# Optimization experiments

Hardware: AMD Instinct MI355X
Metric: run time of the kernel (lower is better)

## Reference

```python
import jax, jax.numpy as jnp
import numpy as np

N_NODES = 50000
N_EDGES = 800000
D_IN = 128
D_OUT = 128


def setup_inputs() -> dict:
    key = jax.random.key(0)
    k1, k2, k3, k4, k5, k6 = jax.random.split(key, 6)
    feat = jax.random.normal(k1, (N_NODES, D_IN), dtype=jnp.float32)
    src = jax.random.randint(k2, (N_EDGES,), 0, N_NODES, dtype=jnp.int64)
    dst = jax.random.randint(k3, (N_EDGES,), 0, N_NODES, dtype=jnp.int64)
    edge_weight = jax.random.uniform(k4, (N_EDGES,), dtype=jnp.float32)
    W_neigh = jax.random.normal(k5, (D_OUT, D_IN), dtype=jnp.float32) * (1.0 / np.sqrt(D_IN))
    W_self = jax.random.normal(k6, (D_OUT, D_IN), dtype=jnp.float32) * (1.0 / np.sqrt(D_IN))
    b_self = jnp.zeros((D_OUT,), dtype=jnp.float32)
    return {"feat": feat, "src": src, "dst": dst, "edge_weight": edge_weight,
            "W_neigh": W_neigh, "W_self": W_self, "b_self": b_self}


def reference(feat, src, dst, edge_weight, W_neigh, W_self, b_self):
    n_nodes = feat.shape[0]
    # fc_neigh on source features: [N, D_out]
    h = feat @ W_neigh.T
    # per-edge weighted messages: m_e = h[src_e] * w_e  -> [E, D_out]
    msg = h[src] * edge_weight[:, None]
    # mean aggregation over incoming edges (0 for isolated dst nodes, as DGL)
    neigh_sum = jax.ops.segment_sum(msg, dst, num_segments=n_nodes)
    deg = jax.ops.segment_sum(jnp.ones_like(edge_weight), dst, num_segments=n_nodes)
    neigh = neigh_sum / jnp.maximum(deg, 1.0)[:, None]
    # fc_self residual path + neighborhood term
    out = feat @ W_self.T + b_self + neigh
    return out
```

## Files before the change

### kernel.cpp

```cpp
#include <hip/hip_runtime.h>

#define CAP 32
#define OVFCAP 65536
#define BSTRIDE 5120
#define BINCHUNK 4096

typedef __attribute__((ext_vector_type(8))) short bf16x8;
typedef __attribute__((ext_vector_type(4))) float f32x4;

__device__ __forceinline__ unsigned f2bf(float x) {
  unsigned u = __float_as_uint(x);
  return (u + 0x7fffu + ((u >> 16) & 1u)) >> 16;
}

__device__ __forceinline__ bf16x8 u4_to_bf(uint4 v) {
  union { uint4 u; bf16x8 b; } cv;
  cv.u = v;
  return cv.b;
}

__global__ __launch_bounds__(512) void zero_kernel(int* __restrict__ p) {
  if (threadIdx.x < 257) p[threadIdx.x] = 0;
}

__global__ __launch_bounds__(256) void prep_kernel(
    const int* __restrict__ src, const int* __restrict__ dst,
    const float* __restrict__ ew, int* __restrict__ gbin,
    uint2* __restrict__ binbuf, int* __restrict__ ovfcnt,
    uint2* __restrict__ ovf, int E,
    const float* __restrict__ feat, unsigned* __restrict__ fb,
    unsigned* __restrict__ fbq, int total4,
    const float* __restrict__ Ws, const float* __restrict__ Wn,
    unsigned* __restrict__ wsb, unsigned* __restrict__ wnb,
    int nchunk) {
  __shared__ int lcnt[256];
  __shared__ int lbase[256];
  const int b = blockIdx.x;
  const int tid = threadIdx.x;
  if (b < nchunk) {
    lcnt[tid] = 0;
    __syncthreads();
    const int e0 = b * BINCHUNK;
    const int e1 = min(E, e0 + BINCHUNK);
    int dreg[BINCHUNK / 256];
#pragma unroll
    for (int i = 0; i < BINCHUNK / 256; ++i) {
      const int e = e0 + i * 256 + tid;
      dreg[i] = (e < e1) ? dst[e] : -1;
      if (dreg[i] >= 0) atomicAdd(&lcnt[dreg[i] >> 8], 1);
    }
    __syncthreads();
    lbase[tid] = lcnt[tid] ? atomicAdd(&gbin[tid], lcnt[tid]) : 0;
    lcnt[tid] = 0;
    __syncthreads();
#pragma unroll
    for (int i = 0; i < BINCHUNK / 256; ++i) {
      const int e = e0 + i * 256 + tid;
      if (e < e1) {
        const int d = dreg[i];
        const int bn = d >> 8;
        const int r = atomicAdd(&lcnt[bn], 1);
        const int pos = lbase[bn] + r;
        const uint2 rec = make_uint2(((unsigned)d << 16) | (unsigned)src[e],
                                     __float_as_uint(ew[e]));
        if (pos < BSTRIDE) {
          binbuf[(size_t)bn * BSTRIDE + pos] = rec;
        } else {
          int p = atomicAdd(ovfcnt, 1);
          if (p < OVFCAP) ovf[p] = rec;
        }
      }
    }
  } else if (b < nchunk + 1024) {
    const int bid = b - nchunk;
    for (int i = bid * 256 + tid; i < total4; i += 1024 * 256) {
      float4 v = ((const float4*)feat)[i];
      fb[2 * i] = f2bf(v.x) | (f2bf(v.y) << 16);
      fb[2 * i + 1] = f2bf(v.z) | (f2bf(v.w) << 16);
      unsigned q = 0;
      q = __builtin_amdgcn_cvt_pk_fp8_f32(v.x, v.y, q, false);
      q = __builtin_amdgcn_cvt_pk_fp8_f32(v.z, v.w, q, true);
      fbq[i] = q;
    }
  } else {
    const int i = (b - nchunk - 1024) * 256 + tid;
    if (i < 8192) {
      float2 a = ((const float2*)Ws)[i];
      wsb[i] = f2bf(a.x) | (f2bf(a.y) << 16);
      float2 v = ((const float2*)Wn)[i];
      wnb[i] = f2bf(v.x) | (f2bf(v.y) << 16);
    }
  }
}

__global__ __launch_bounds__(256) void bucket_kernel(
    const int* __restrict__ gbin, const uint2* __restrict__ binbuf,
    int* __restrict__ cnt, unsigned* __restrict__ colw,
    int* __restrict__ ovfcnt, uint2* __restrict__ ovf, int n) {
  __shared__ uint4 lbucket4[256 * CAP / 4];
  __shared__ int lcnt[256];
  unsigned* lbucket = (unsigned*)lbucket4;
  const int b = blockIdx.x;
  const int tid = threadIdx.x;
  lcnt[tid] = 0;
  __syncthreads();
  const int lo = b << 8;
  const int m = min(gbin[b], BSTRIDE);
  const uint2* bb = binbuf + (size_t)b * BSTRIDE;
  for (int i = tid; i < m; i += 256) {
    const uint2 rec = bb[i];
    const int dl = (int)(rec.x >> 16) & 255;
    const int r = atomicAdd(&lcnt[dl], 1);
    if (r < CAP) {
      const float w = __uint_as_float(rec.y);
      const unsigned q = (unsigned)(w * 65535.0f + 0.5f);
      lbucket[dl * CAP + r] = ((rec.x & 0xffffu) << 16) | q;
    } else {
      int p = atomicAdd(ovfcnt, 1);
      if (p < OVFCAP) ovf[p] = rec;
    }
  }
  __syncthreads();
  const int nn = min(256, n - lo);
  if (tid < nn) cnt[lo + tid] = lcnt[tid];
  const int tot4 = (nn * CAP) >> 2;
  uint4* d4 = (uint4*)(colw + (size_t)lo * CAP);
  for (int i = tid; i < tot4; i += 256) d4[i] = lbucket4[i];
}

__global__ __launch_bounds__(256) void gather_kernel(
    const unsigned* __restrict__ fbq, const int* __restrict__ cnt,
    const unsigned* __restrict__ colw, const int* __restrict__ ovfcnt,
    const uint2* __restrict__ ovf, unsigned* __restrict__ aggu, int n) {
  const int wid = (blockIdx.x * 256 + threadIdx.x) >> 6;
  const int lane = threadIdx.x & 63;
  if (wid >= n) return;
  const int g = lane >> 5;
  const int sl = lane & 31;
  const int dg = cnt[wid];
  const int m = min(dg, CAP);
  const unsigned pv = (lane < m) ? colw[(size_t)wid * CAP + lane] : 0u;
  float a0 = 0.f, a1 = 0.f, a2 = 0.f, a3 = 0.f;
  const float qs = 1.0f / 65535.0f;
  int t = 0;
  for (; t + 16 <= m; t += 16) {
    unsigned p[8], u[8];
#pragma unroll
    for (int i = 0; i < 8; ++i) p[i] = __shfl(pv, t + 2 * i + g);
#pragma unroll
    for (int i = 0; i < 8; ++i) u[i] = fbq[(size_t)(p[i] >> 16) * 32 + sl];
#pragma unroll
    for (int i = 0; i < 8; ++i) {
      const float w = (float)(p[i] & 0xffffu) * qs;
      a0 += __builtin_amdgcn_cvt_f32_fp8(u[i], 0) * w;
      a1 += __builtin_amdgcn_cvt_f32_fp8(u[i], 1) * w;
      a2 += __builtin_amdgcn_cvt_f32_fp8(u[i], 2) * w;
      a3 += __builtin_amdgcn_cvt_f32_fp8(u[i], 3) * w;
    }
  }
  if (t + 8 <= m) {
    unsigned p[4], u[4];
#pragma unroll
    for (int i = 0; i < 4; ++i) p[i] = __shfl(pv, t + 2 * i + g);
#pragma unroll
    for (int i = 0; i < 4; ++i) u[i] = fbq[(size_t)(p[i] >> 16) * 32 + sl];
#pragma unroll
    for (int i = 0; i < 4; ++i) {
      const float w = (float)(p[i] & 0xffffu) * qs;
      a0 += __builtin_amdgcn_cvt_f32_fp8(u[i], 0) * w;
      a1 += __builtin_amdgcn_cvt_f32_fp8(u[i], 1) * w;
      a2 += __builtin_amdgcn_cvt_f32_fp8(u[i], 2) * w;
      a3 += __builtin_amdgcn_cvt_f32_fp8(u[i], 3) * w;
    }
    t += 8;
  }
  for (; t + 2 <= m; t += 2) {
    const unsigned p = __shfl(pv, t + g);
    const unsigned u = fbq[(size_t)(p >> 16) * 32 + sl];
    const float w = (float)(p & 0xffffu) * qs;
    a0 += __builtin_amdgcn_cvt_f32_fp8(u, 0) * w;
    a1 += __builtin_amdgcn_cvt_f32_fp8(u, 1) * w;
    a2 += __builtin_amdgcn_cvt_f32_fp8(u, 2) * w;
    a3 += __builtin_amdgcn_cvt_f32_fp8(u, 3) * w;
  }
  if (t < m && g == 0) {
    const unsigned p = __shfl(pv, t);
    const unsigned u = fbq[(size_t)(p >> 16) * 32 + sl];
    const float w = (float)(p & 0xffffu) * qs;
    a0 += __builtin_amdgcn_cvt_f32_fp8(u, 0) * w;
    a1 += __builtin_amdgcn_cvt_f32_fp8(u, 1) * w;
    a2 += __builtin_amdgcn_cvt_f32_fp8(u, 2) * w;
    a3 += __builtin_amdgcn_cvt_f32_fp8(u, 3) * w;
  }
  const int novf = min(*ovfcnt, OVFCAP);
  if (novf > 0 && g == 0) {
    for (int i = 0; i < novf; ++i) {
      const uint2 v = ovf[i];
      if ((int)(v.x >> 16) == wid) {
        const unsigned u = fbq[(size_t)(v.x & 0xffffu) * 32 + sl];
        const float w = __uint_as_float(v.y);
        a0 += __builtin_amdgcn_cvt_f32_fp8(u, 0) * w;
        a1 += __builtin_amdgcn_cvt_f32_fp8(u, 1) * w;
        a2 += __builtin_amdgcn_cvt_f32_fp8(u, 2) * w;
        a3 += __builtin_amdgcn_cvt_f32_fp8(u, 3) * w;
      }
    }
  }
  const int peer = (lane + 32) & 63;
  const float b0 = __shfl(a0, peer);
  const float b1 = __shfl(a1, peer);
  const float b2 = __shfl(a2, peer);
  const float b3 = __shfl(a3, peer);
  if (g == 0) {
    const float sc = 1.0f / fmaxf((float)dg, 1.0f);
    const float c0 = (a0 + b0) * sc, c1 = (a1 + b1) * sc;
    const float c2 = (a2 + b2) * sc, c3 = (a3 + b3) * sc;
    uint2 o;
    o.x = f2bf(c0) | (f2bf(c1) << 16);
    o.y = f2bf(c2) | (f2bf(c3) << 16);
    *(uint2*)(aggu + (size_t)wid * 128 + 2 * sl) = o;
  }
}

__global__ __launch_bounds__(256) void fused_gemm_kernel(
    const ushort* __restrict__ fb,
    const unsigned* __restrict__ aggu,
    const uint4* __restrict__ ws4,
    const uint4* __restrict__ wn4,
    const float* __restrict__ bsv,
    float* __restrict__ out,
    int n) {
  __shared__ uint4 wlds[128 * 32];
  const int tid = threadIdx.x;
  for (int i = tid; i < 2048; i += 256) {
    const int c = i >> 4, s = i & 15;
    const int sw = s ^ (c & 7);
    wlds[c * 32 + sw] = ws4[i];
    wlds[c * 32 + 16 + sw] = wn4[i];
  }
  __syncthreads();

  const int lane = tid & 63;
  const int wv = tid >> 6;
  const int row0 = (blockIdx.x * 4 + wv) * 32;
  if (row0 >= n) return;
  const int rlo = lane & 15;
  const int g = lane >> 4;

  f32x4 acc0[8], acc1[8];
#pragma unroll
  for (int ct = 0; ct < 8; ++ct) {
    const float bv = bsv[ct * 16 + rlo];
    acc0[ct] = (f32x4){bv, bv, bv, bv};
    acc1[ct] = (f32x4){bv, bv, bv, bv};
  }

  const int rA0 = min(row0 + rlo, n - 1);
  const int rA1 = min(row0 + 16 + rlo, n - 1);
  const int x7 = rlo & 7;

#pragma unroll
  for (int kc = 0; kc < 4; ++kc) {
    const int k0 = kc * 32 + g * 8;
    const bf16x8 as0 = *(const bf16x8*)(fb + (size_t)rA0 * 128 + k0);
    const bf16x8 ag0 = *(const bf16x8*)(aggu + (size_t)rA0 * 128 + (k0 >> 1));
    const bf16x8 as1 = *(const bf16x8*)(fb + (size_t)rA1 * 128 + k0);
    const bf16x8 ag1 = *(const bf16x8*)(aggu + (size_t)rA1 * 128 + (k0 >> 1));
    const int slot = (kc * 4 + g) ^ x7;
#pragma unroll
    for (int ct = 0; ct < 8; ++ct) {
      const int c = ct * 16 + rlo;
      const bf16x8 bsw = u4_to_bf(wlds[c * 32 + slot]);
      const bf16x8 bnw = u4_to_bf(wlds[c * 32 + 16 + slot]);
      acc0[ct] = __builtin_amdgcn_mfma_f32_16x16x32_bf16(as0, bsw, acc0[ct], 0, 0, 0);
      acc0[ct] = __builtin_amdgcn_mfma_f32_16x16x32_bf16(ag0, bnw, acc0[ct], 0, 0, 0);
      acc1[ct] = __builtin_amdgcn_mfma_f32_16x16x32_bf16(as1, bsw, acc1[ct], 0, 0, 0);
      acc1[ct] = __builtin_amdgcn_mfma_f32_16x16x32_bf16(ag1, bnw, acc1[ct], 0, 0, 0);
    }
  }

#pragma unroll
  for (int ct = 0; ct < 8; ++ct) {
#pragma unroll
    for (int j = 0; j < 4; ++j) {
      const int r0 = row0 + g * 4 + j;
      if (r0 < n) out[(size_t)r0 * 128 + ct * 16 + rlo] = acc0[ct][j];
      const int r1 = row0 + 16 + g * 4 + j;
      if (r1 < n) out[(size_t)r1 * 128 + ct * 16 + rlo] = acc1[ct][j];
    }
  }
}

extern "C" void kernel_launch(void* const* d_in, const int* in_sizes, int n_in,
                              void* d_out, int out_size, void* d_ws, size_t ws_size,
                              hipStream_t stream) {
  const float* feat = (const float*)d_in[0];
  const int* src = (const int*)d_in[1];
  const int* dst = (const int*)d_in[2];
  const float* ew = (const float*)d_in[3];
  const float* Wn = (const float*)d_in[4];
  const float* Ws = (const float*)d_in[5];
  const float* bs = (const float*)d_in[6];
  const int n = in_sizes[0] / 128;
  const int E = in_sizes[1];
  float* out = (float*)d_out;
  unsigned* aggu = (unsigned*)d_out;

  const int nbins = (n + 255) >> 8;

  char* w = (char*)d_ws;
  size_t off_colw = 0;
  size_t off_cnt = (off_colw + (size_t)n * CAP * 4 + 255) & ~(size_t)255;
  size_t off_ovf = (off_cnt + (size_t)(n + 1 + 256) * 4 + 255) & ~(size_t)255;
  size_t off_binbuf = (off_ovf + (size_t)OVFCAP * 8 + 255) & ~(size_t)255;
  size_t off_fb = (off_binbuf + (size_t)256 * BSTRIDE * 8 + 255) & ~(size_t)255;
  size_t off_fbq = (off_fb + (size_t)n * 64 * 4 + 255) & ~(size_t)255;
  size_t off_wsb = (off_fbq + (size_t)n * 32 * 4 + 255) & ~(size_t)255;
  size_t off_wnb = off_wsb + 8192 * 4;
  unsigned* colw = (unsigned*)(w + off_colw);
  int* cnt = (int*)(w + off_cnt);
  int* ovfcnt = cnt + n;
  int* gbin = cnt + n + 1;
  uint2* ovf = (uint2*)(w + off_ovf);
  uint2* binbuf = (uint2*)(w + off_binbuf);
  unsigned* fb = (unsigned*)(w + off_fb);
  unsigned* fbq = (unsigned*)(w + off_fbq);
  unsigned* wsb = (unsigned*)(w + off_wsb);
  unsigned* wnb = (unsigned*)(w + off_wnb);

  zero_kernel<<<1, 512, 0, stream>>>(ovfcnt);

  const int nchunk = (E + BINCHUNK - 1) / BINCHUNK;
  prep_kernel<<<nchunk + 1024 + 32, 256, 0, stream>>>(
      src, dst, ew, gbin, binbuf, ovfcnt, ovf, E,
      feat, fb, fbq, n * 32, Ws, Wn, wsb, wnb, nchunk);

  bucket_kernel<<<nbins, 256, 0, stream>>>(gbin, binbuf, cnt, colw, ovfcnt, ovf, n);

  gather_kernel<<<(n * 64 + 255) / 256, 256, 0, stream>>>(
      fbq, cnt, colw, ovfcnt, ovf, aggu, n);

  const int nblocks = (n + 127) / 128;
  fused_gemm_kernel<<<nblocks, 256, 0, stream>>>(
      (const ushort*)fb, aggu, (const uint4*)wsb, (const uint4*)wnb, bs, out, n);
}
```

Baseline: 75.62 us.

## Split fp8 features into two column planes and gather per plane; shrink dst bins

The fp8 feature copy is stored as two 64-column planes. The gather runs twice, once per plane, with four edge groups of 16 lanes per wave instead of two groups of 32, so each pass touches a half-size feature working set that fits cache better. Binning moves from 256-node to 64-node bins, which gives more bucket blocks and a smaller LDS footprint per block, and the binning kernel tracks up to 1024 bin counters. The cost is a second gather launch that rereads the CSR and ovf data, plus an extra cross-lane reduction step.

Result: slower. 89.65 us (+18.5%).

```diff
diff --git a/kernel.cpp b/kernel.cpp
--- a/kernel.cpp
+++ b/kernel.cpp
@@ -2,7 +2,8 @@
 
 #define CAP 32
 #define OVFCAP 65536
-#define BSTRIDE 5120
+#define NBIN_SH 6
+#define BSTRIDE 1280
 #define BINCHUNK 4096
 
 typedef __attribute__((ext_vector_type(8))) short bf16x8;
@@ -19,8 +20,8 @@
   return cv.b;
 }
 
-__global__ __launch_bounds__(512) void zero_kernel(int* __restrict__ p) {
-  if (threadIdx.x < 257) p[threadIdx.x] = 0;
+__global__ __launch_bounds__(1024) void zero_kernel(int* __restrict__ p, int cnt) {
+  if ((int)threadIdx.x < cnt) p[threadIdx.x] = 0;
 }
 
 __global__ __launch_bounds__(256) void prep_kernel(
@@ -29,16 +30,16 @@
     uint2* __restrict__ binbuf, int* __restrict__ ovfcnt,
     uint2* __restrict__ ovf, int E,
     const float* __restrict__ feat, unsigned* __restrict__ fb,
-    unsigned* __restrict__ fbq, int total4,
+    unsigned* __restrict__ fbq, int n,
     const float* __restrict__ Ws, const float* __restrict__ Wn,
     unsigned* __restrict__ wsb, unsigned* __restrict__ wnb,
-    int nchunk) {
-  __shared__ int lcnt[256];
-  __shared__ int lbase[256];
+    int nchunk, int nbins) {
+  __shared__ int lcnt[1024];
+  __shared__ int lbase[1024];
   const int b = blockIdx.x;
   const int tid = threadIdx.x;
   if (b < nchunk) {
-    lcnt[tid] = 0;
+    for (int i = tid; i < nbins; i += 256) lcnt[i] = 0;
     __syncthreads();
     const int e0 = b * BINCHUNK;
     const int e1 = min(E, e0 + BINCHUNK);
@@ -47,18 +48,20 @@
     for (int i = 0; i < BINCHUNK / 256; ++i) {
       const int e = e0 + i * 256 + tid;
       dreg[i] = (e < e1) ? dst[e] : -1;
-      if (dreg[i] >= 0) atomicAdd(&lcnt[dreg[i] >> 8], 1);
+      if (dreg[i] >= 0) atomicAdd(&lcnt[dreg[i] >> NBIN_SH], 1);
     }
     __syncthreads();
-    lbase[tid] = lcnt[tid] ? atomicAdd(&gbin[tid], lcnt[tid]) : 0;
-    lcnt[tid] = 0;
+    for (int i = tid; i < nbins; i += 256) {
+      lbase[i] = lcnt[i] ? atomicAdd(&gbin[i], lcnt[i]) : 0;
+      lcnt[i] = 0;
+    }
     __syncthreads();
 #pragma unroll
     for (int i = 0; i < BINCHUNK / 256; ++i) {
       const int e = e0 + i * 256 + tid;
       if (e < e1) {
         const int d = dreg[i];
-        const int bn = d >> 8;
+        const int bn = d >> NBIN_SH;
         const int r = atomicAdd(&lcnt[bn], 1);
         const int pos = lbase[bn] + r;
         const uint2 rec = make_uint2(((unsigned)d << 16) | (unsigned)src[e],
@@ -73,6 +76,8 @@
     }
   } else if (b < nchunk + 1024) {
     const int bid = b - nchunk;
+    const int total4 = n * 32;
+    const size_t n16 = (size_t)n * 16;
     for (int i = bid * 256 + tid; i < total4; i += 1024 * 256) {
       float4 v = ((const float4*)feat)[i];
       fb[2 * i] = f2bf(v.x) | (f2bf(v.y) << 16);
@@ -80,7 +85,8 @@
       unsigned q = 0;
       q = __builtin_amdgcn_cvt_pk_fp8_f32(v.x, v.y, q, false);
       q = __builtin_amdgcn_cvt_pk_fp8_f32(v.z, v.w, q, true);
-      fbq[i] = q;
+      const int node = i >> 5, j = i & 31;
+      fbq[(size_t)(j >> 4) * n16 + (size_t)node * 16 + (j & 15)] = q;
     }
   } else {
     const int i = (b - nchunk - 1024) * 256 + tid;
@@ -97,19 +103,19 @@
     const int* __restrict__ gbin, const uint2* __restrict__ binbuf,
     int* __restrict__ cnt, unsigned* __restrict__ colw,
     int* __restrict__ ovfcnt, uint2* __restrict__ ovf, int n) {
-  __shared__ uint4 lbucket4[256 * CAP / 4];
-  __shared__ int lcnt[256];
+  __shared__ uint4 lbucket4[64 * CAP / 4];
+  __shared__ int lcnt[64];
   unsigned* lbucket = (unsigned*)lbucket4;
   const int b = blockIdx.x;
   const int tid = threadIdx.x;
-  lcnt[tid] = 0;
+  if (tid < 64) lcnt[tid] = 0;
   __syncthreads();
-  const int lo = b << 8;
+  const int lo = b << NBIN_SH;
   const int m = min(gbin[b], BSTRIDE);
   const uint2* bb = binbuf + (size_t)b * BSTRIDE;
   for (int i = tid; i < m; i += 256) {
     const uint2 rec = bb[i];
-    const int dl = (int)(rec.x >> 16) & 255;
+    const int dl = (int)(rec.x >> 16) & 63;
     const int r = atomicAdd(&lcnt[dl], 1);
     if (r < CAP) {
       const float w = __uint_as_float(rec.y);
@@ -121,7 +127,7 @@
     }
   }
   __syncthreads();
-  const int nn = min(256, n - lo);
+  const int nn = min(64, n - lo);
   if (tid < nn) cnt[lo + tid] = lcnt[tid];
   const int tot4 = (nn * CAP) >> 2;
   uint4* d4 = (uint4*)(colw + (size_t)lo * CAP);
@@ -129,14 +135,16 @@
 }
 
 __global__ __launch_bounds__(256) void gather_kernel(
-    const unsigned* __restrict__ fbq, const int* __restrict__ cnt,
+    const unsigned* __restrict__ fbqp,
+    const int* __restrict__ cnt,
     const unsigned* __restrict__ colw, const int* __restrict__ ovfcnt,
-    const uint2* __restrict__ ovf, unsigned* __restrict__ aggu, int n) {
+    const uint2* __restrict__ ovf, unsigned* __restrict__ aggu,
+    int n, int plane) {
   const int wid = (blockIdx.x * 256 + threadIdx.x) >> 6;
   const int lane = threadIdx.x & 63;
   if (wid >= n) return;
-  const int g = lane >> 5;
-  const int sl = lane & 31;
+  const int g = lane >> 4;
+  const int sl = lane & 15;
   const int dg = cnt[wid];
   const int m = min(dg, CAP);
   const unsigned pv = (lane < m) ? colw[(size_t)wid * CAP + lane] : 0u;
@@ -144,26 +152,11 @@
   const float qs = 1.0f / 65535.0f;
   int t = 0;
   for (; t + 16 <= m; t += 16) {
-    unsigned p[8], u[8];
-#pragma unroll
-    for (int i = 0; i < 8; ++i) p[i] = __shfl(pv, t + 2 * i + g);
-#pragma unroll
-    for (int i = 0; i < 8; ++i) u[i] = fbq[(size_t)(p[i] >> 16) * 32 + sl];
-#pragma unroll
-    for (int i = 0; i < 8; ++i) {
-      const float w = (float)(p[i] & 0xffffu) * qs;
-      a0 += __builtin_amdgcn_cvt_f32_fp8(u[i], 0) * w;
-      a1 += __builtin_amdgcn_cvt_f32_fp8(u[i], 1) * w;
-      a2 += __builtin_amdgcn_cvt_f32_fp8(u[i], 2) * w;
-      a3 += __builtin_amdgcn_cvt_f32_fp8(u[i], 3) * w;
-    }
-  }
-  if (t + 8 <= m) {
     unsigned p[4], u[4];
 #pragma unroll
-    for (int i = 0; i < 4; ++i) p[i] = __shfl(pv, t + 2 * i + g);
-#pragma unroll
-    for (int i = 0; i < 4; ++i) u[i] = fbq[(size_t)(p[i] >> 16) * 32 + sl];
+    for (int i = 0; i < 4; ++i) p[i] = __shfl(pv, t + 4 * i + g);
+#pragma unroll
+    for (int i = 0; i < 4; ++i) u[i] = fbqp[(size_t)(p[i] >> 16) * 16 + sl];
 #pragma unroll
     for (int i = 0; i < 4; ++i) {
       const float w = (float)(p[i] & 0xffffu) * qs;
@@ -172,21 +165,22 @@
       a2 += __builtin_amdgcn_cvt_f32_fp8(u[i], 2) * w;
       a3 += __builtin_amdgcn_cvt_f32_fp8(u[i], 3) * w;
     }
-    t += 8;
-  }
-  for (; t + 2 <= m; t += 2) {
+  }
+  for (; t + 4 <= m; t += 4) {
     const unsigned p = __shfl(pv, t + g);
-    const unsigned u = fbq[(size_t)(p >> 16) * 32 + sl];
+    const unsigned u = fbqp[(size_t)(p >> 16) * 16 + sl];
     const float w = (float)(p & 0xffffu) * qs;
     a0 += __builtin_amdgcn_cvt_f32_fp8(u, 0) * w;
     a1 += __builtin_amdgcn_cvt_f32_fp8(u, 1) * w;
     a2 += __builtin_amdgcn_cvt_f32_fp8(u, 2) * w;
     a3 += __builtin_amdgcn_cvt_f32_fp8(u, 3) * w;
   }
-  if (t < m && g == 0) {
-    const unsigned p = __shfl(pv, t);
-    const unsigned u = fbq[(size_t)(p >> 16) * 32 + sl];
-    const float w = (float)(p & 0xffffu) * qs;
+  if (t < m) {
+    const int rem = m - t;
+    const int gi = (g < rem) ? g : 0;
+    const unsigned p = __shfl(pv, t + gi);
+    const float w = (g < rem) ? (float)(p & 0xffffu) * qs : 0.0f;
+    const unsigned u = fbqp[(size_t)(p >> 16) * 16 + sl];
     a0 += __builtin_amdgcn_cvt_f32_fp8(u, 0) * w;
     a1 += __builtin_amdgcn_cvt_f32_fp8(u, 1) * w;
     a2 += __builtin_amdgcn_cvt_f32_fp8(u, 2) * w;
@@ -197,7 +191,7 @@
     for (int i = 0; i < novf; ++i) {
       const uint2 v = ovf[i];
       if ((int)(v.x >> 16) == wid) {
-        const unsigned u = fbq[(size_t)(v.x & 0xffffu) * 32 + sl];
+        const unsigned u = fbqp[(size_t)(v.x & 0xffffu) * 16 + sl];
         const float w = __uint_as_float(v.y);
         a0 += __builtin_amdgcn_cvt_f32_fp8(u, 0) * w;
         a1 += __builtin_amdgcn_cvt_f32_fp8(u, 1) * w;
@@ -206,19 +200,17 @@
       }
     }
   }
-  const int peer = (lane + 32) & 63;
-  const float b0 = __shfl(a0, peer);
-  const float b1 = __shfl(a1, peer);
-  const float b2 = __shfl(a2, peer);
-  const float b3 = __shfl(a3, peer);
+  a0 += __shfl_xor(a0, 16); a0 += __shfl_xor(a0, 32);
+  a1 += __shfl_xor(a1, 16); a1 += __shfl_xor(a1, 32);
+  a2 += __shfl_xor(a2, 16); a2 += __shfl_xor(a2, 32);
+  a3 += __shfl_xor(a3, 16); a3 += __shfl_xor(a3, 32);
   if (g == 0) {
     const float sc = 1.0f / fmaxf((float)dg, 1.0f);
-    const float c0 = (a0 + b0) * sc, c1 = (a1 + b1) * sc;
-    const float c2 = (a2 + b2) * sc, c3 = (a3 + b3) * sc;
+    const float c0 = a0 * sc, c1 = a1 * sc, c2 = a2 * sc, c3 = a3 * sc;
     uint2 o;
     o.x = f2bf(c0) | (f2bf(c1) << 16);
     o.y = f2bf(c2) | (f2bf(c3) << 16);
-    *(uint2*)(aggu + (size_t)wid * 128 + 2 * sl) = o;
+    *(uint2*)(aggu + (size_t)wid * 128 + plane * 32 + 2 * sl) = o;
   }
 }
 
@@ -306,14 +298,14 @@
   float* out = (float*)d_out;
   unsigned* aggu = (unsigned*)d_out;
 
-  const int nbins = (n + 255) >> 8;
+  const int nbins = (n + 63) >> NBIN_SH;
 
   char* w = (char*)d_ws;
   size_t off_colw = 0;
   size_t off_cnt = (off_colw + (size_t)n * CAP * 4 + 255) & ~(size_t)255;
-  size_t off_ovf = (off_cnt + (size_t)(n + 1 + 256) * 4 + 255) & ~(size_t)255;
+  size_t off_ovf = (off_cnt + (size_t)(n + 1 + 1024) * 4 + 255) & ~(size_t)255;
   size_t off_binbuf = (off_ovf + (size_t)OVFCAP * 8 + 255) & ~(size_t)255;
-  size_t off_fb = (off_binbuf + (size_t)256 * BSTRIDE * 8 + 255) & ~(size_t)255;
+  size_t off_fb = (off_binbuf + (size_t)nbins * BSTRIDE * 8 + 255) & ~(size_t)255;
   size_t off_fbq = (off_fb + (size_t)n * 64 * 4 + 255) & ~(size_t)255;
   size_t off_wsb = (off_fbq + (size_t)n * 32 * 4 + 255) & ~(size_t)255;
   size_t off_wnb = off_wsb + 8192 * 4;
@@ -328,17 +320,19 @@
   unsigned* wsb = (unsigned*)(w + off_wsb);
   unsigned* wnb = (unsigned*)(w + off_wnb);
 
-  zero_kernel<<<1, 512, 0, stream>>>(ovfcnt);
+  zero_kernel<<<1, 1024, 0, stream>>>(ovfcnt, 1 + nbins);
 
   const int nchunk = (E + BINCHUNK - 1) / BINCHUNK;
   prep_kernel<<<nchunk + 1024 + 32, 256, 0, stream>>>(
       src, dst, ew, gbin, binbuf, ovfcnt, ovf, E,
-      feat, fb, fbq, n * 32, Ws, Wn, wsb, wnb, nchunk);
+      feat, fb, fbq, n, Ws, Wn, wsb, wnb, nchunk, nbins);
 
   bucket_kernel<<<nbins, 256, 0, stream>>>(gbin, binbuf, cnt, colw, ovfcnt, ovf, n);
 
-  gather_kernel<<<(n * 64 + 255) / 256, 256, 0, stream>>>(
-      fbq, cnt, colw, ovfcnt, ovf, aggu, n);
+  const size_t n16 = (size_t)n * 16;
+  const int gblocks = (n * 64 + 255) / 256;
+  gather_kernel<<<gblocks, 256, 0, stream>>>(fbq, cnt, colw, ovfcnt, ovf, aggu, n, 0);
+  gather_kernel<<<gblocks, 256, 0, stream>>>(fbq + n16, cnt, colw, ovfcnt, ovf, aggu, n, 1);
 
   const int nblocks = (n + 127) / 128;
   fused_gemm_kernel<<<nblocks, 256, 0, stream>>>(
```
